# Kernel tuning notes

Measured on AMD Instinct MI355X. Metric: run time of the kernel, lower is better.

The kernel has to match this reference:

```python
import jax, jax.numpy as jnp
import numpy as np

N = 50000
E = 800000
HIGH, LOW, EMB = 128, 32, 64
HID, HEADS, OUT = 32, 8, 8
IN1 = HIGH + EMB  # 192
IN2 = HID * HEADS  # 256
NEG_SLOPE = 0.2


def setup_inputs() -> dict:
    key = jax.random.key(0)
    ks = jax.random.split(key, 12)
    s = lambda k, shape: (jax.random.normal(k, shape, dtype=jnp.float32) * 0.1)
    return {
        "high_dim_features": jax.random.normal(ks[0], (N, HIGH), dtype=jnp.float32),
        "low_dim_features": jax.random.normal(ks[1], (N, LOW), dtype=jnp.float32),
        "edge_index": jax.random.randint(ks[2], (2, E), 0, N, dtype=jnp.int32),
        "W_emb": s(ks[3], (LOW, EMB)),
        "b_emb": jnp.zeros((EMB,), jnp.float32),
        "W1": s(ks[4], (IN1, HEADS * HID)),
        "att_src1": s(ks[5], (HEADS, HID)),
        "att_dst1": s(ks[6], (HEADS, HID)),
        "b1": jnp.zeros((HEADS * HID,), jnp.float32),
        "W2": s(ks[7], (IN2, OUT)),
        "att_src2": s(ks[8], (1, OUT)),
        "att_dst2": s(ks[9], (1, OUT)),
        "b2": jnp.zeros((OUT,), jnp.float32),
    }


def _gat_layer(x, src, dst, W, att_src, att_dst, bias, heads, out_ch, concat):
    # x: [N, F_in]; src/dst: [E'] (self-loops already appended)
    n = x.shape[0]
    h = (x @ W).reshape(n, heads, out_ch)            # [N, H, C]
    a_src = jnp.einsum('nhc,hc->nh', h, att_src)     # [N, H]
    a_dst = jnp.einsum('nhc,hc->nh', h, att_dst)
    alpha = a_src[src] + a_dst[dst]                  # [E', H]
    alpha = jax.nn.leaky_relu(alpha, NEG_SLOPE)
    # segment softmax over incoming edges per destination node
    m = jax.ops.segment_max(alpha, dst, num_segments=n)
    ea = jnp.exp(alpha - m[dst])
    z = jax.ops.segment_sum(ea, dst, num_segments=n)
    alpha = ea / (z[dst] + 1e-16)                    # [E', H]
    msg = h[src] * alpha[:, :, None]                 # [E', H, C]
    out = jax.ops.segment_sum(msg, dst, num_segments=n)  # [N, H, C]
    if concat:
        out = out.reshape(n, heads * out_ch)
    else:
        out = out.mean(axis=1)
    return out + bias


def reference(high_dim_features, low_dim_features, edge_index,
              W_emb, b_emb, W1, att_src1, att_dst1, b1,
              W2, att_src2, att_dst2, b2):
    # embedding + elu, concat
    emb = jax.nn.elu(low_dim_features @ W_emb + b_emb)
    x = jnp.concatenate([high_dim_features, emb], axis=1)  # [N, IN1]
    # add self-loops (PyG default)
    loops = jnp.arange(N, dtype=edge_index.dtype)
    src = jnp.concatenate([edge_index[0], loops])
    dst = jnp.concatenate([edge_index[1], loops])
    x = _gat_layer(x, src, dst, W1, att_src1, att_dst1, b1, HEADS, HID, True)
    x = jax.nn.elu(x)  # dropout: eval mode no-op
    x = _gat_layer(x, src, dst, W2, att_src2, att_dst2, b2, 1, OUT, False)
    return jax.nn.log_softmax(x, axis=1)
```

## Files before the change

kernel.cpp:

```cpp
#include <hip/hip_runtime.h>
#include <hip/hip_bf16.h>

typedef __hip_bfloat16 bf16;
typedef short bf16x8 __attribute__((ext_vector_type(8)));
typedef float f32x4  __attribute__((ext_vector_type(4)));

__device__ __forceinline__ float bf2f(bf16 v){ return __bfloat162float(v); }
__device__ __forceinline__ bf16  f2bf(float f){ return __float2bfloat16(f); }
__device__ __forceinline__ float lrelu(float a){ return a > 0.f ? a : 0.2f*a; }
__device__ __forceinline__ float bfbits(short s){
    union{unsigned u; float f;} cv; cv.u = ((unsigned)(unsigned short)s) << 16; return cv.f;
}
__device__ __forceinline__ short bf16s(float f){ bf16 q = f2bf(f); return *(short*)&q; }
__device__ __forceinline__ float cvtf(const void* p, int i, int isb){
    return isb ? bf2f(((const bf16*)p)[i]) : ((const float*)p)[i];
}
__device__ __forceinline__ short cvts(const void* p, int i, int isb){
    return isb ? ((const short*)p)[i] : bf16s(((const float*)p)[i]);
}
__device__ __forceinline__ bf16x8 load8(const void* base, size_t off, int isb){
    if (isb) return *(const bf16x8*)((const bf16*)base + off);
    const float* f = (const float*)base + off;
    f32x4 v0 = *(const f32x4*)f;
    f32x4 v1 = *(const f32x4*)(f + 4);
    short r[8];
    #pragma unroll
    for (int j = 0; j < 4; j++) r[j]   = bf16s(v0[j]);
    #pragma unroll
    for (int j = 0; j < 4; j++) r[4+j] = bf16s(v1[j]);
    return *(const bf16x8*)r;
}

__global__ void k_detect(const unsigned short* __restrict__ raw, int* __restrict__ flag){
    int t = threadIdx.x;
    unsigned short w = raw[2*t];
    int e = (w >> 7) & 0xFF;
    int ok = (e >= 90 && e <= 140) ? 1 : 0;
    __shared__ int cnt;
    if (t == 0) cnt = 0;
    __syncthreads();
    atomicAdd(&cnt, ok);
    __syncthreads();
    if (t == 0) *flag = (cnt >= 192) ? 1 : 0;
}

__global__ __launch_bounds__(256) void k_prep(const void* __restrict__ low,
        const void* __restrict__ Wemb, const void* __restrict__ bemb,
        const void* __restrict__ W1, const void* __restrict__ W2,
        bf16* __restrict__ emb, bf16* __restrict__ Bp, bf16* __restrict__ Bp2,
        const int* __restrict__ ei, int* __restrict__ counts,
        const int* __restrict__ flag, int N, int E, int nEmb, int nPack, int nCnt){
    __shared__ float wem[2048 + 64];
    __shared__ short lows[1024];
    int t = threadIdx.x;
    int b = blockIdx.x;
    int isb = *flag;
    if (b >= nEmb + nPack){
        int cb = b - nEmb - nPack;
        int ET = E + N;
        for (int i = cb*256 + t; i < ET; i += nCnt*256){
            int dst = (i < E) ? ei[E + i] : (i - E);
            atomicAdd(&counts[dst], 1);
        }
        return;
    }
    if (b >= nEmb){
        int i = (b - nEmb)*256 + t;
        if (i < 16*6*64*8){
            int j = i & 7;
            int lane = (i >> 3) & 63;
            int r = i >> 9;
            int kt = r % 6, nt = r / 6;
            int k = kt*32 + (lane >> 4)*8 + j;
            int n = nt*16 + (lane & 15);
            *(short*)&Bp[i] = cvts(W1, k*256 + n, isb);
        } else {
            int i2 = i - 16*6*64*8;
            if (i2 >= 8*64*8) return;
            int j = i2 & 7;
            int lane = (i2 >> 3) & 63;
            int kt = i2 >> 9;
            int k = kt*32 + (lane >> 4)*8 + j;
            int n = lane & 15;
            *(short*)&Bp2[i2] = (n < 8) ? cvts(W2, k*8 + n, isb) : (short)0;
        }
        return;
    }
    int nb0 = b * 32;
    for (int i = t; i < 2048; i += 256) wem[i] = cvtf(Wemb, i, isb);
    if (t < 64) wem[2048 + t] = cvtf(bemb, t, isb);
    int lim = (N - nb0) * 32; if (lim > 1024) lim = 1024;
    for (int i = t; i < 1024; i += 256)
        lows[i] = (i < lim) ? cvts(low, nb0*32 + i, isb) : (short)0;
    __syncthreads();
    int nl = t >> 3, j8 = (t & 7) * 8;
    float acc[8];
    #pragma unroll
    for (int j = 0; j < 8; j++) acc[j] = wem[2048 + j8 + j];
    for (int k = 0; k < 32; k++){
        float lv = bfbits(lows[nl*32 + k]);
        f32x4 w0 = *(const f32x4*)&wem[k*64 + j8];
        f32x4 w1 = *(const f32x4*)&wem[k*64 + j8 + 4];
        #pragma unroll
        for (int j = 0; j < 4; j++) acc[j]   += lv * w0[j];
        #pragma unroll
        for (int j = 0; j < 4; j++) acc[4+j] += lv * w1[j];
    }
    int n = nb0 + nl;
    if (n < N){
        short ov[8];
        #pragma unroll
        for (int j = 0; j < 8; j++){
            float v = acc[j];
            ov[j] = bf16s(v > 0.f ? v : expm1f(v));
        }
        *(bf16x8*)&emb[(size_t)n*64 + j8] = *(const bf16x8*)ov;
    }
}

__global__ __launch_bounds__(256) void k_scan_local(const int* __restrict__ counts,
        int* __restrict__ rowptr, int* __restrict__ partials, int N){
    __shared__ int sd[256];
    int t = threadIdx.x;
    int i = blockIdx.x*256 + t;
    int v = (i < N) ? counts[i] : 0;
    sd[t] = v;
    __syncthreads();
    #pragma unroll
    for (int off = 1; off < 256; off <<= 1){
        int a = (t >= off) ? sd[t - off] : 0;
        __syncthreads();
        sd[t] += a;
        __syncthreads();
    }
    if (i < N) rowptr[i] = sd[t] - v;
    if (t == 255) partials[blockIdx.x] = sd[255];
}

__global__ __launch_bounds__(256) void k_scan_part(int* __restrict__ partials,
        int* __restrict__ blockoff, int* __restrict__ rowptrN, int NB){
    __shared__ int sd[256];
    __shared__ int carry;
    int t = threadIdx.x;
    if (t == 0) carry = 0;
    __syncthreads();
    for (int base = 0; base < NB; base += 256){
        int i = base + t;
        int v = (i < NB) ? partials[i] : 0;
        sd[t] = v;
        __syncthreads();
        #pragma unroll
        for (int off = 1; off < 256; off <<= 1){
            int a = (t >= off) ? sd[t - off] : 0;
            __syncthreads();
            sd[t] += a;
            __syncthreads();
        }
        if (i < NB) blockoff[i] = carry + sd[t] - v;
        __syncthreads();
        if (t == 255) carry += sd[255];
        __syncthreads();
    }
    if (t == 0) *rowptrN = carry;
}

__global__ void k_scan_add(int* __restrict__ rowptr, int* __restrict__ cursor,
        const int* __restrict__ blockoff, int N){
    int i = blockIdx.x*256 + threadIdx.x;
    if (i < N){
        int r = rowptr[i] + blockoff[i >> 8];
        rowptr[i] = r;
        cursor[i] = r;
    }
}

__global__ void k_scatter(const int* __restrict__ ei, int E, int N,
        int* __restrict__ cursor, int* __restrict__ srcs){
    int i = blockIdx.x*256 + threadIdx.x;
    int tot = E + N;
    if (i < tot){
        int src, dst;
        if (i < E){ src = ei[i]; dst = ei[E + i]; }
        else      { src = i - E; dst = i - E; }
        int pos = atomicAdd(&cursor[dst], 1);
        srcs[pos] = src;
    }
}

__global__ __launch_bounds__(256, 3) void k_gemm1(const void* __restrict__ highv,
        const bf16* __restrict__ emb, const bf16* __restrict__ Bp,
        const void* __restrict__ attS, const void* __restrict__ attD,
        bf16* __restrict__ h1, float* __restrict__ a_s, float* __restrict__ a_d,
        const int* __restrict__ flag, int N){
    const int RS = 260;
    __shared__ float eb[16*260 + 16];
    __shared__ float att[512];
    int t = threadIdx.x;
    int isb = *flag;
    att[t] = cvtf(attS, t, isb);
    att[256 + t] = cvtf(attD, t, isb);
    int w = t >> 6, lane = t & 63;
    int m_lo = lane & 15, quad = lane >> 4;
    int m0 = blockIdx.x * 64;
    int mr[4];
    #pragma unroll
    for (int rt = 0; rt < 4; rt++){
        int m = m0 + rt*16 + m_lo;
        mr[rt] = m < N ? m : N-1;
    }
    f32x4 acc[4][4];
    #pragma unroll
    for (int rt = 0; rt < 4; rt++)
        #pragma unroll
        for (int ct = 0; ct < 4; ct++) acc[rt][ct] = (f32x4){0.f,0.f,0.f,0.f};

    #pragma unroll 2
    for (int kt = 0; kt < 6; kt++){
        bf16x8 a[4], b[4];
        if (kt < 4){
            #pragma unroll
            for (int rt = 0; rt < 4; rt++)
                a[rt] = load8(highv, (size_t)mr[rt]*128 + kt*32 + quad*8, isb);
        } else {
            #pragma unroll
            for (int rt = 0; rt < 4; rt++)
                a[rt] = *(const bf16x8*)&emb[(size_t)mr[rt]*64 + (kt-4)*32 + quad*8];
        }
        #pragma unroll
        for (int ct = 0; ct < 4; ct++)
            b[ct] = *(const bf16x8*)&Bp[(size_t)(((w*4 + ct)*6 + kt)*64 + lane)*8];
        #pragma unroll
        for (int rt = 0; rt < 4; rt++)
            #pragma unroll
            for (int ct = 0; ct < 4; ct++)
                acc[rt][ct] = __builtin_amdgcn_mfma_f32_16x16x32_bf16(a[rt], b[ct], acc[rt][ct], 0, 0, 0);
    }

    #pragma unroll 1
    for (int rt = 0; rt < 4; rt++){
        __syncthreads();
        #pragma unroll
        for (int ct = 0; ct < 4; ct++)
            #pragma unroll
            for (int reg = 0; reg < 4; reg++)
                eb[(quad*4 + reg)*RS + w*64 + ct*16 + m_lo] = acc[rt][ct][reg];
        __syncthreads();
        int r = t >> 4, cb = t & 15;
        int c0 = cb * 16;
        int m = m0 + rt*16 + r;
        f32x4 v[4];
        #pragma unroll
        for (int p = 0; p < 4; p++) v[p] = *(const f32x4*)&eb[r*RS + c0 + p*4];
        float ps = 0.f, pd = 0.f;
        #pragma unroll
        for (int p = 0; p < 4; p++)
            #pragma unroll
            for (int j = 0; j < 4; j++){
                ps += v[p][j] * att[c0 + p*4 + j];
                pd += v[p][j] * att[256 + c0 + p*4 + j];
            }
        if (m < N){
            short ov[16];
            #pragma unroll
            for (int p = 0; p < 4; p++)
                #pragma unroll
                for (int j = 0; j < 4; j++) ov[p*4+j] = bf16s(v[p][j]);
            *(bf16x8*)&h1[(size_t)m*256 + c0]     = *(const bf16x8*)&ov[0];
            *(bf16x8*)&h1[(size_t)m*256 + c0 + 8] = *(const bf16x8*)&ov[8];
        }
        ps += __shfl_xor(ps, 1);
        pd += __shfl_xor(pd, 1);
        if (((t & 1) == 0) && m < N){
            int hd = cb >> 1;
            a_s[m*8 + hd] = ps;
            a_d[m*8 + hd] = pd;
        }
    }
}

__global__ __launch_bounds__(256) void k_edge1(const int* __restrict__ rowptr,
        const int* __restrict__ srcs, const float* __restrict__ a_s,
        const float* __restrict__ a_d, const bf16* __restrict__ h1,
        const void* __restrict__ b1, bf16* __restrict__ x2,
        const int* __restrict__ flag, int N){
    int t = threadIdx.x;
    int lane = t & 63, wv = t >> 6;
    int n = blockIdx.x*4 + wv;
    if (n >= N) return;
    int beg = rowptr[n];
    int deg = rowptr[n+1] - beg;

    int cl = lane & 31;
    int hb = cl >> 2;
    int half = lane >> 5;
    float adb = a_d[n*8 + hb];

    float acc[8];
    #pragma unroll
    for (int j = 0; j < 8; j++) acc[j] = 0.f;
    float z = 0.f;

    int e = half;
    for (; e + 6 < deg; e += 8){
        int s0 = srcs[beg + e];
        int s1 = srcs[beg + e + 2];
        int s2 = srcs[beg + e + 4];
        int s3 = srcs[beg + e + 6];
        float w0 = __expf(fminf(lrelu(a_s[s0*8 + hb] + adb), 80.f));
        float w1 = __expf(fminf(lrelu(a_s[s1*8 + hb] + adb), 80.f));
        float w2 = __expf(fminf(lrelu(a_s[s2*8 + hb] + adb), 80.f));
        float w3 = __expf(fminf(lrelu(a_s[s3*8 + hb] + adb), 80.f));
        bf16x8 v0 = *(const bf16x8*)&h1[(size_t)s0*256 + cl*8];
        bf16x8 v1 = *(const bf16x8*)&h1[(size_t)s1*256 + cl*8];
        bf16x8 v2 = *(const bf16x8*)&h1[(size_t)s2*256 + cl*8];
        bf16x8 v3 = *(const bf16x8*)&h1[(size_t)s3*256 + cl*8];
        z += (w0 + w1) + (w2 + w3);
        #pragma unroll
        for (int j = 0; j < 8; j++) acc[j] += w0 * bfbits(v0[j]);
        #pragma unroll
        for (int j = 0; j < 8; j++) acc[j] += w1 * bfbits(v1[j]);
        #pragma unroll
        for (int j = 0; j < 8; j++) acc[j] += w2 * bfbits(v2[j]);
        #pragma unroll
        for (int j = 0; j < 8; j++) acc[j] += w3 * bfbits(v3[j]);
    }
    for (; e < deg; e += 2){
        int s = srcs[beg + e];
        float w = __expf(fminf(lrelu(a_s[s*8 + hb] + adb), 80.f));
        bf16x8 hv = *(const bf16x8*)&h1[(size_t)s*256 + cl*8];
        z += w;
        #pragma unroll
        for (int j = 0; j < 8; j++) acc[j] += w * bfbits(hv[j]);
    }
    #pragma unroll
    for (int j = 0; j < 8; j++) acc[j] += __shfl_xor(acc[j], 32);
    z += __shfl_xor(z, 32);
    float rz = 1.f / (z + 1e-16f);

    if (half == 0){
        int isb = *flag;
        bf16x8 bv = load8(b1, cl*8, isb);
        short ov[8];
        #pragma unroll
        for (int j = 0; j < 8; j++){
            float v = acc[j] * rz + bfbits(bv[j]);
            ov[j] = bf16s(v > 0.f ? v : expm1f(v));
        }
        *(bf16x8*)&x2[(size_t)n*256 + cl*8] = *(const bf16x8*)ov;
    }
}

__global__ __launch_bounds__(256) void k_gemm2(const bf16* __restrict__ x2,
        const bf16* __restrict__ Bp2, const void* __restrict__ attS,
        const void* __restrict__ attD, float* __restrict__ h2,
        float* __restrict__ a2s, float* __restrict__ a2d,
        const int* __restrict__ flag, int N){
    int t = threadIdx.x;
    int isb = *flag;
    int w = t >> 6, lane = t & 63;
    int m_lo = lane & 15, quad = lane >> 4;
    int m0 = blockIdx.x*64 + w*16;
    int mr = m0 + m_lo; if (mr >= N) mr = N-1;
    f32x4 acc = (f32x4){0.f,0.f,0.f,0.f};
    #pragma unroll
    for (int kt = 0; kt < 8; kt++){
        bf16x8 a = *(const bf16x8*)&x2[(size_t)mr*256 + kt*32 + quad*8];
        bf16x8 b = *(const bf16x8*)&Bp2[(size_t)(kt*64 + lane)*8];
        acc = __builtin_amdgcn_mfma_f32_16x16x32_bf16(a, b, acc, 0, 0, 0);
    }
    float s2 = (m_lo < 8) ? cvtf(attS, m_lo, isb) : 0.f;
    float d2 = (m_lo < 8) ? cvtf(attD, m_lo, isb) : 0.f;
    #pragma unroll
    for (int reg = 0; reg < 4; reg++){
        int m = m0 + quad*4 + reg;
        float val = acc[reg];
        float ps = val * s2, pd = val * d2;
        ps += __shfl_xor(ps, 1); ps += __shfl_xor(ps, 2);
        ps += __shfl_xor(ps, 4); ps += __shfl_xor(ps, 8);
        pd += __shfl_xor(pd, 1); pd += __shfl_xor(pd, 2);
        pd += __shfl_xor(pd, 4); pd += __shfl_xor(pd, 8);
        if (m < N){
            if (m_lo < 8) h2[(size_t)m*8 + m_lo] = val;
            if (m_lo == 0){ a2s[m] = ps; a2d[m] = pd; }
        }
    }
}

__global__ __launch_bounds__(256) void k_edge2(const int* __restrict__ rowptr,
        const int* __restrict__ srcs, const float* __restrict__ a2s,
        const float* __restrict__ a2d, const float* __restrict__ h2,
        const void* __restrict__ b2, void* __restrict__ outv,
        const int* __restrict__ flag, int N){
    int t = threadIdx.x;
    int lane = t & 63, wv = t >> 6;
    int n = blockIdx.x*4 + wv;
    if (n >= N) return;
    int beg = rowptr[n];
    int deg = rowptr[n+1] - beg;
    float adh = a2d[n];
    int ep = lane >> 3, c = lane & 7;
    float acc = 0.f, z = 0.f;
    for (int e = ep; e < deg; e += 8){
        int s = srcs[beg + e];
        float w = __expf(fminf(lrelu(a2s[s] + adh), 80.f));
        z += w;
        acc += w * h2[(size_t)s*8 + c];
    }
    acc += __shfl_xor(acc, 8);
    acc += __shfl_xor(acc, 16);
    acc += __shfl_xor(acc, 32);
    z += __shfl_xor(z, 8);
    z += __shfl_xor(z, 16);
    z += __shfl_xor(z, 32);
    int isb = *flag;
    float val = acc / (z + 1e-16f) + cvtf(b2, c, isb);
    float mx = val;
    mx = fmaxf(mx, __shfl_xor(mx, 1));
    mx = fmaxf(mx, __shfl_xor(mx, 2));
    mx = fmaxf(mx, __shfl_xor(mx, 4));
    float se = __expf(val - mx);
    se += __shfl_xor(se, 1); se += __shfl_xor(se, 2); se += __shfl_xor(se, 4);
    float r = val - mx - __logf(se);
    if (lane < 8){
        if (isb) ((bf16*)outv)[(size_t)n*8 + c] = f2bf(r);
        else     ((float*)outv)[(size_t)n*8 + c] = r;
    }
}

extern "C" void kernel_launch(void* const* d_in, const int* in_sizes, int n_in,
                              void* d_out, int out_size, void* d_ws, size_t ws_size,
                              hipStream_t stream) {
    const int* ei = (const int*)d_in[2];
    const int N = in_sizes[0] / 128;
    const int E = in_sizes[2] / 2;
    const int ET = E + N;
    const int NB = (N + 255) / 256;

    char* p = (char*)d_ws;
    auto alloc = [&](size_t bytes) -> void* {
        char* r = p;
        p += (bytes + 255) & ~(size_t)255;
        return (void*)r;
    };
    int*   flag     = (int*)  alloc(256);
    int*   counts   = (int*)  alloc((size_t)N*4);
    int*   rowptr   = (int*)  alloc((size_t)(N+1)*4);
    int*   cursor   = (int*)  alloc((size_t)N*4);
    int*   srcs     = (int*)  alloc((size_t)ET*4);
    int*   partials = (int*)  alloc((size_t)NB*4);
    int*   blockoff = (int*)  alloc((size_t)NB*4);
    bf16*  Bp       = (bf16*) alloc((size_t)192*256*2);
    bf16*  Bp2      = (bf16*) alloc((size_t)8*64*8*2);
    bf16*  emb      = (bf16*) alloc((size_t)N*64*2);
    bf16*  h1       = (bf16*) alloc((size_t)N*256*2);
    float* a_s      = (float*)alloc((size_t)N*8*4);
    float* a_d      = (float*)alloc((size_t)N*8*4);
    bf16*  x2       = (bf16*) alloc((size_t)N*256*2);
    float* h2       = (float*)alloc((size_t)N*8*4);
    float* a2s      = (float*)alloc((size_t)N*4);
    float* a2d      = (float*)alloc((size_t)N*4);

    k_detect<<<1, 256, 0, stream>>>((const unsigned short*)d_in[0], flag);
    hipMemsetAsync(counts, 0, (size_t)N*4, stream);

    {
        int nEmb  = (N + 31)/32;
        int nPack = (16*6*64*8 + 8*64*8 + 255)/256;
        int nCnt  = 1024;
        k_prep<<<nEmb + nPack + nCnt, 256, 0, stream>>>(d_in[1], d_in[3], d_in[4],
                d_in[5], d_in[9], emb, Bp, Bp2, ei, counts, flag, N, E, nEmb, nPack, nCnt);
    }
    k_scan_local<<<NB, 256, 0, stream>>>(counts, rowptr, partials, N);
    k_scan_part <<<1, 256, 0, stream>>>(partials, blockoff, rowptr + N, NB);
    k_scan_add  <<<NB, 256, 0, stream>>>(rowptr, cursor, blockoff, N);
    k_scatter<<<(ET + 255)/256, 256, 0, stream>>>(ei, E, N, cursor, srcs);
    k_gemm1<<<(N + 63)/64, 256, 0, stream>>>(d_in[0], emb, Bp, d_in[6], d_in[7],
                                             h1, a_s, a_d, flag, N);
    k_edge1<<<(N + 3)/4, 256, 0, stream>>>(rowptr, srcs, a_s, a_d, h1, d_in[8], x2, flag, N);
    k_gemm2<<<(N + 63)/64, 256, 0, stream>>>(x2, Bp2, d_in[10], d_in[11], h2, a2s, a2d, flag, N);
    k_edge2<<<(N + 3)/4, 256, 0, stream>>>(rowptr, srcs, a2s, a2d, h2, d_in[12], d_out, flag, N);
}
```

Before: 372.2 us.

## Fuse layer-2 projection into edge1 epilogue and merge scan kernels

The layer-2 linear projection and its attention logits are now computed inside the layer-1 aggregation kernel, straight from the per-node activations held in registers. This drops the x2 intermediate (N×256 bf16 written and read back) and one kernel launch. Separately, the two-pass scan finish (single-block partial scan plus add pass) becomes one kernel in which every block rescans the partial sums itself. The cost is that W2 is read through scalar loads with per-element conversion in each wave, plus extra shuffle reductions, instead of an MFMA GEMM.

```diff
diff --git a/kernel.cpp b/kernel.cpp
--- a/kernel.cpp
+++ b/kernel.cpp
@@ -137,41 +137,37 @@
     if (t == 255) partials[blockIdx.x] = sd[255];
 }
 
-__global__ __launch_bounds__(256) void k_scan_part(int* __restrict__ partials,
-        int* __restrict__ blockoff, int* __restrict__ rowptrN, int NB){
+__global__ __launch_bounds__(256) void k_scan_fin(const int* __restrict__ partials,
+        int* __restrict__ rowptr, int* __restrict__ cursor, int N, int NB){
     __shared__ int sd[256];
-    __shared__ int carry;
-    int t = threadIdx.x;
-    if (t == 0) carry = 0;
-    __syncthreads();
+    int b = blockIdx.x, t = threadIdx.x;
+    int off = 0, total = 0;
     for (int base = 0; base < NB; base += 256){
-        int i = base + t;
-        int v = (i < NB) ? partials[i] : 0;
+        int v = (base + t < NB) ? partials[base + t] : 0;
+        __syncthreads();
         sd[t] = v;
         __syncthreads();
         #pragma unroll
-        for (int off = 1; off < 256; off <<= 1){
-            int a = (t >= off) ? sd[t - off] : 0;
+        for (int o2 = 1; o2 < 256; o2 <<= 1){
+            int a = (t >= o2) ? sd[t - o2] : 0;
             __syncthreads();
             sd[t] += a;
             __syncthreads();
         }
-        if (i < NB) blockoff[i] = carry + sd[t] - v;
-        __syncthreads();
-        if (t == 255) carry += sd[255];
-        __syncthreads();
-    }
-    if (t == 0) *rowptrN = carry;
-}
-
-__global__ void k_scan_add(int* __restrict__ rowptr, int* __restrict__ cursor,
-        const int* __restrict__ blockoff, int N){
-    int i = blockIdx.x*256 + threadIdx.x;
+        if (b >= base && b < base + 256){
+            int idx = b - base;
+            int local = (idx == 0) ? 0 : sd[idx - 1];
+            off = total + local;
+        }
+        total += sd[255];
+    }
+    int i = b*256 + t;
     if (i < N){
-        int r = rowptr[i] + blockoff[i >> 8];
+        int r = rowptr[i] + off;
         rowptr[i] = r;
         cursor[i] = r;
     }
+    if (b == NB-1 && t == 255) rowptr[N] = total;
 }
 
 __global__ void k_scatter(const int* __restrict__ ei, int E, int N,
@@ -281,12 +277,15 @@
 __global__ __launch_bounds__(256) void k_edge1(const int* __restrict__ rowptr,
         const int* __restrict__ srcs, const float* __restrict__ a_s,
         const float* __restrict__ a_d, const bf16* __restrict__ h1,
-        const void* __restrict__ b1, bf16* __restrict__ x2,
+        const void* __restrict__ b1, const void* __restrict__ W2,
+        const void* __restrict__ attS2, const void* __restrict__ attD2,
+        float* __restrict__ h2, float* __restrict__ a2s, float* __restrict__ a2d,
         const int* __restrict__ flag, int N){
     int t = threadIdx.x;
     int lane = t & 63, wv = t >> 6;
     int n = blockIdx.x*4 + wv;
     if (n >= N) return;
+    int isb = *flag;
     int beg = rowptr[n];
     int deg = rowptr[n+1] - beg;
 
@@ -337,53 +336,41 @@
     z += __shfl_xor(z, 32);
     float rz = 1.f / (z + 1e-16f);
 
-    if (half == 0){
-        int isb = *flag;
-        bf16x8 bv = load8(b1, cl*8, isb);
-        short ov[8];
-        #pragma unroll
-        for (int j = 0; j < 8; j++){
-            float v = acc[j] * rz + bfbits(bv[j]);
-            ov[j] = bf16s(v > 0.f ? v : expm1f(v));
-        }
-        *(bf16x8*)&x2[(size_t)n*256 + cl*8] = *(const bf16x8*)ov;
-    }
-}
-
-__global__ __launch_bounds__(256) void k_gemm2(const bf16* __restrict__ x2,
-        const bf16* __restrict__ Bp2, const void* __restrict__ attS,
-        const void* __restrict__ attD, float* __restrict__ h2,
-        float* __restrict__ a2s, float* __restrict__ a2d,
-        const int* __restrict__ flag, int N){
-    int t = threadIdx.x;
-    int isb = *flag;
-    int w = t >> 6, lane = t & 63;
-    int m_lo = lane & 15, quad = lane >> 4;
-    int m0 = blockIdx.x*64 + w*16;
-    int mr = m0 + m_lo; if (mr >= N) mr = N-1;
-    f32x4 acc = (f32x4){0.f,0.f,0.f,0.f};
-    #pragma unroll
-    for (int kt = 0; kt < 8; kt++){
-        bf16x8 a = *(const bf16x8*)&x2[(size_t)mr*256 + kt*32 + quad*8];
-        bf16x8 b = *(const bf16x8*)&Bp2[(size_t)(kt*64 + lane)*8];
-        acc = __builtin_amdgcn_mfma_f32_16x16x32_bf16(a, b, acc, 0, 0, 0);
-    }
-    float s2 = (m_lo < 8) ? cvtf(attS, m_lo, isb) : 0.f;
-    float d2 = (m_lo < 8) ? cvtf(attD, m_lo, isb) : 0.f;
-    #pragma unroll
-    for (int reg = 0; reg < 4; reg++){
-        int m = m0 + quad*4 + reg;
-        float val = acc[reg];
-        float ps = val * s2, pd = val * d2;
-        ps += __shfl_xor(ps, 1); ps += __shfl_xor(ps, 2);
-        ps += __shfl_xor(ps, 4); ps += __shfl_xor(ps, 8);
-        pd += __shfl_xor(pd, 1); pd += __shfl_xor(pd, 2);
-        pd += __shfl_xor(pd, 4); pd += __shfl_xor(pd, 8);
-        if (m < N){
-            if (m_lo < 8) h2[(size_t)m*8 + m_lo] = val;
-            if (m_lo == 0){ a2s[m] = ps; a2d[m] = pd; }
-        }
-    }
+    bf16x8 bv = load8(b1, cl*8, isb);
+    float x2v[8];
+    #pragma unroll
+    for (int j = 0; j < 8; j++){
+        float v = acc[j] * rz + bfbits(bv[j]);
+        x2v[j] = v > 0.f ? v : expm1f(v);
+    }
+    float p[4];
+    #pragma unroll
+    for (int o = 0; o < 4; o++){
+        int oo = half*4 + o;
+        float s = 0.f;
+        #pragma unroll
+        for (int j = 0; j < 8; j++)
+            s += x2v[j] * cvtf(W2, (cl*8 + j)*8 + oo, isb);
+        p[o] = s;
+    }
+    #pragma unroll
+    for (int m = 1; m < 32; m <<= 1){
+        #pragma unroll
+        for (int o = 0; o < 4; o++) p[o] += __shfl_xor(p[o], m);
+    }
+    if (cl == 0){
+        f32x4 hv = {p[0], p[1], p[2], p[3]};
+        *(f32x4*)&h2[(size_t)n*8 + half*4] = hv;
+    }
+    float ps = 0.f, pd = 0.f;
+    #pragma unroll
+    for (int o = 0; o < 4; o++){
+        ps += p[o] * cvtf(attS2, half*4 + o, isb);
+        pd += p[o] * cvtf(attD2, half*4 + o, isb);
+    }
+    ps += __shfl_xor(ps, 32);
+    pd += __shfl_xor(pd, 32);
+    if (lane == 0){ a2s[n] = ps; a2d[n] = pd; }
 }
 
 __global__ __launch_bounds__(256) void k_edge2(const int* __restrict__ rowptr,
@@ -448,14 +435,12 @@
     int*   cursor   = (int*)  alloc((size_t)N*4);
     int*   srcs     = (int*)  alloc((size_t)ET*4);
     int*   partials = (int*)  alloc((size_t)NB*4);
-    int*   blockoff = (int*)  alloc((size_t)NB*4);
     bf16*  Bp       = (bf16*) alloc((size_t)192*256*2);
     bf16*  Bp2      = (bf16*) alloc((size_t)8*64*8*2);
     bf16*  emb      = (bf16*) alloc((size_t)N*64*2);
     bf16*  h1       = (bf16*) alloc((size_t)N*256*2);
     float* a_s      = (float*)alloc((size_t)N*8*4);
     float* a_d      = (float*)alloc((size_t)N*8*4);
-    bf16*  x2       = (bf16*) alloc((size_t)N*256*2);
     float* h2       = (float*)alloc((size_t)N*8*4);
     float* a2s      = (float*)alloc((size_t)N*4);
     float* a2d      = (float*)alloc((size_t)N*4);
@@ -471,12 +456,12 @@
                 d_in[5], d_in[9], emb, Bp, Bp2, ei, counts, flag, N, E, nEmb, nPack, nCnt);
     }
     k_scan_local<<<NB, 256, 0, stream>>>(counts, rowptr, partials, N);
-    k_scan_part <<<1, 256, 0, stream>>>(partials, blockoff, rowptr + N, NB);
-    k_scan_add  <<<NB, 256, 0, stream>>>(rowptr, cursor, blockoff, N);
+    k_scan_fin  <<<NB, 256, 0, stream>>>(partials, rowptr, cursor, N, NB);
     k_scatter<<<(ET + 255)/256, 256, 0, stream>>>(ei, E, N, cursor, srcs);
     k_gemm1<<<(N + 63)/64, 256, 0, stream>>>(d_in[0], emb, Bp, d_in[6], d_in[7],
                                              h1, a_s, a_d, flag, N);
-    k_edge1<<<(N + 3)/4, 256, 0, stream>>>(rowptr, srcs, a_s, a_d, h1, d_in[8], x2, flag, N);
-    k_gemm2<<<(N + 63)/64, 256, 0, stream>>>(x2, Bp2, d_in[10], d_in[11], h2, a2s, a2d, flag, N);
+    k_edge1<<<(N + 3)/4, 256, 0, stream>>>(rowptr, srcs, a_s, a_d, h1, d_in[8],
+                                           d_in[9], d_in[10], d_in[11],
+                                           h2, a2s, a2d, flag, N);
     k_edge2<<<(N + 3)/4, 256, 0, stream>>>(rowptr, srcs, a2s, a2d, h2, d_in[12], d_out, flag, N);
 }
```

New measurement: 509.3 us. 1.37x slower.
